# Kernel tuning notes

Measured on AMD Instinct MI355X. Metric: run time of the kernel, lower is better.

The kernel has to match this reference:

```python
import jax, jax.numpy as jnp
import numpy as np

VAR0, VAR1 = 0.1, 0.2
THRESH = 0.5
NEG_POS = 3
NEG_INF = -1e30


def point_form(b):
    # (cx,cy,w,h) -> (x1,y1,x2,y2)
    return jnp.concatenate([b[..., :2] - b[..., 2:] * 0.5,
                            b[..., :2] + b[..., 2:] * 0.5], -1)


def iou(a, b):
    # a: [G,4], b: [A,4], both xyxy -> [G,A]
    tl = jnp.maximum(a[:, None, :2], b[None, :, :2])
    br = jnp.minimum(a[:, None, 2:], b[None, :, 2:])
    wh = jnp.clip(br - tl, 0.0)
    inter = wh[..., 0] * wh[..., 1]
    area_a = (a[:, 2] - a[:, 0]) * (a[:, 3] - a[:, 1])
    area_b = (b[:, 2] - b[:, 0]) * (b[:, 3] - b[:, 1])
    return inter / (area_a[:, None] + area_b[None, :] - inter)


def encode_single(gt_boxes, gt_labels, anchors):
    # gt_boxes [G,4] xyxy, gt_labels [G], anchors [A,4] cxcywh
    ov = iou(gt_boxes, point_form(anchors))            # [G,A]
    best_prior_idx = jnp.argmax(ov, axis=1)            # [G] guaranteed match
    best_truth_ov = jnp.max(ov, axis=0)                # [A]
    best_truth_idx = jnp.argmax(ov, axis=0)            # [A]
    G = gt_boxes.shape[0]
    best_truth_ov = best_truth_ov.at[best_prior_idx].set(2.0)
    best_truth_idx = best_truth_idx.at[best_prior_idx].set(jnp.arange(G))
    matches = gt_boxes[best_truth_idx]                 # [A,4]
    conf = jnp.where(best_truth_ov < THRESH, 0, gt_labels[best_truth_idx] + 1)
    m_cxcy = (matches[:, :2] + matches[:, 2:]) * 0.5
    m_wh = matches[:, 2:] - matches[:, :2]
    g_cxcy = (m_cxcy - anchors[:, :2]) / (VAR0 * anchors[:, 2:])
    g_wh = jnp.log(m_wh / anchors[:, 2:]) / VAR1
    return conf, jnp.concatenate([g_cxcy, g_wh], -1)


def smooth_l1(d):
    ad = jnp.abs(d)
    return jnp.where(ad < 1.0, 0.5 * d * d, ad - 0.5)


def ssd_guarantee_loss(pred_conf, pred_loc, anchors_b, gt_boxes, gt_labels):
    # anchors_b: per-image anchors [B,A,4] (cxcywh)
    conf_t, loc_t = jax.vmap(encode_single)(gt_boxes, gt_labels, anchors_b)
    loc_t = jax.lax.stop_gradient(loc_t)               # loc_t.detach() in torch
    pos = conf_t > 0                                   # [B,A]
    N = jnp.sum(pos).astype(pred_loc.dtype)
    loc_loss = jnp.sum(jnp.where(pos[..., None], smooth_l1(pred_loc - loc_t), 0.0))
    logp = jax.nn.log_softmax(pred_conf, axis=-1)
    ce = -jnp.take_along_axis(logp, conf_t[..., None], axis=-1)[..., 0]  # [B,A]
    A = pred_conf.shape[1]
    pos_num = jnp.sum(pos, axis=1)                     # [B]
    neg_num = jnp.maximum(10, jnp.minimum(pos_num * NEG_POS, A - pos_num))
    neg_ce = jnp.where(conf_t == 0, ce, NEG_INF)
    neg_sorted = -jnp.sort(-neg_ce, axis=1)            # descending hard-negative sort
    rank = jnp.arange(A)
    take = (rank[None, :] < neg_num[:, None]) & (neg_sorted > 0.5 * NEG_INF)
    class_loss = (jnp.sum(jnp.where(pos, ce, 0.0))
                  + jnp.sum(jnp.where(take, neg_sorted, 0.0))) / N
    return class_loss, loc_loss / N, N


def decode(loc, anchors):
    # loc [B,A,4], anchors [A,4] cxcywh -> refined anchors [B,A,4] cxcywh
    cxcy = anchors[None, :, :2] + loc[..., :2] * VAR0 * anchors[None, :, 2:]
    wh = anchors[None, :, 2:] * jnp.exp(loc[..., 2:] * VAR1)
    return jnp.concatenate([cxcy, wh], -1)


def setup_inputs() -> dict:
    key = jax.random.key(0)
    ks = jax.random.split(key, 10)
    B, A, C, G = 32, 16320, 81, 32
    objectness = jax.random.normal(ks[0], (B, A, 2), jnp.float32)
    refine_loc = 0.1 * jax.random.normal(ks[1], (B, A, 4), jnp.float32)
    pred_conf = jax.random.normal(ks[2], (B, A, C), jnp.float32)
    pred_loc = 0.1 * jax.random.normal(ks[3], (B, A, 4), jnp.float32)
    # anchors: valid normalized cxcywh
    a_cxcy = 0.05 + 0.9 * jax.random.uniform(ks[4], (1, A, 2), jnp.float32)
    a_wh = 0.02 + 0.23 * jax.random.uniform(ks[5], (1, A, 2), jnp.float32)
    anchors = jnp.concatenate([a_cxcy, a_wh], -1)
    # gt boxes: valid xyxy in [0,1]
    g_cxcy = 0.2 + 0.6 * jax.random.uniform(ks[6], (B, G, 2), jnp.float32)
    g_wh = 0.05 + 0.25 * jax.random.uniform(ks[7], (B, G, 2), jnp.float32)
    gt_boxes = jnp.clip(jnp.concatenate([g_cxcy - g_wh * 0.5, g_cxcy + g_wh * 0.5], -1), 0.0, 1.0)
    gt_labels = jax.random.randint(ks[8], (B, G), 0, C - 1, jnp.int32)
    return {"objectness": objectness, "refine_loc": refine_loc, "pred_conf": pred_conf,
            "pred_loc": pred_loc, "anchors": anchors, "gt_boxes": gt_boxes,
            "gt_labels": gt_labels}


def reference(objectness, refine_loc, pred_conf, pred_loc, anchors, gt_boxes, gt_labels):
    a0 = anchors[0]                                    # [A,4]
    B = pred_conf.shape[0]
    anchors_b = jnp.broadcast_to(a0, (B,) + a0.shape)
    # ARM: binary objectness, labels zeroed
    arm_cls, arm_loc, _ = ssd_guarantee_loss(objectness, refine_loc, anchors_b,
                                             gt_boxes, jnp.zeros_like(gt_labels))
    # ODM: match against per-image refined anchors
    refined = decode(refine_loc, a0)
    odm_cls, odm_loc, _ = ssd_guarantee_loss(pred_conf, pred_loc, refined,
                                             gt_boxes, gt_labels)
    total = arm_cls + arm_loc + odm_cls + odm_loc
    return (total, odm_cls, odm_loc, arm_cls, arm_loc)
```

## Files before the change

### kernel.cpp

```cpp
#include <hip/hip_runtime.h>
#include <hip/hip_bf16.h>

constexpr int NB = 32;
constexpr int NA = 16320;
constexpr int NG = 32;
constexpr int NC = 81;
constexpr int LSE_BLKS = 2048;
constexpr int CE_BLKS = 2040;

__device__ __forceinline__ float sl1(float d) {
    float ad = fabsf(d);
    return ad < 1.f ? 0.5f * d * d : ad - 0.5f;
}

__device__ __forceinline__ unsigned long long umax64(unsigned long long a, unsigned long long b) {
    return a > b ? a : b;
}

__global__ __launch_bounds__(256) void k_mega(
    const float* __restrict__ anchors,
    const float* __restrict__ refine_loc,
    const float* __restrict__ gt_boxes,
    const float* __restrict__ pred_conf,
    float* __restrict__ lse,
    float* __restrict__ ws_ov,
    unsigned char* __restrict__ ws_idx,
    unsigned long long* __restrict__ ws_part)
{
    __shared__ float4 s_gt[NG];
    __shared__ float s_ga[NG];
    __shared__ unsigned long long s_part[4][NG];

    int bid = blockIdx.x;
    int q = bid / 3, r3 = bid - q * 3;
    int tid = threadIdx.x;

    if (r3 == 0) {
        int lane = tid & 63, sub = lane & 7, grp = lane >> 3;
        int wid = q * 4 + (tid >> 6);
        const int NWAVE = LSE_BLKS * 4;
        const int TOT = NB * NA / 8;
        float x[11]; int idx;
        {
            idx = wid * 8 + grp;
            const float* p = pred_conf + (size_t)idx * NC;
            #pragma unroll
            for (int j = 0; j < 10; j++) x[j] = p[sub + 8 * j];
            x[10] = (sub == 0) ? p[80] : -87.f;
        }
        for (int gi = wid; gi < TOT; gi += NWAVE) {
            float y[11]; int idy = 0;
            int nx = gi + NWAVE;
            if (nx < TOT) {
                idy = nx * 8 + grp;
                const float* p = pred_conf + (size_t)idy * NC;
                #pragma unroll
                for (int j = 0; j < 10; j++) y[j] = p[sub + 8 * j];
                y[10] = (sub == 0) ? p[80] : -87.f;
            } else {
                #pragma unroll
                for (int j = 0; j < 11; j++) y[j] = -87.f;
            }
            float s = __expf(x[10]);
            #pragma unroll
            for (int j = 0; j < 10; j++) s += __expf(x[j]);
            s += __shfl_xor(s, 1);
            s += __shfl_xor(s, 2);
            s += __shfl_xor(s, 4);
            if (sub == 0) lse[idx] = __logf(s);
            #pragma unroll
            for (int j = 0; j < 11; j++) x[j] = y[j];
            idx = idy;
        }
        return;
    }

    int mb = 2 * q + (r3 - 1);
    int row = mb >> 6, chunk = mb & 63;
    int lossId = row >> 5, b = row & 31;
    if (tid < NG) {
        float4 g = *(const float4*)&gt_boxes[(size_t)(b * NG + tid) * 4];
        s_gt[tid] = g;
        s_ga[tid] = (g.z - g.x) * (g.w - g.y);
    }
    __syncthreads();
    int a = chunk * 256 + tid;
    bool valid = a < NA;
    int al = valid ? a : NA - 1;
    float4 an = *(const float4*)&anchors[(size_t)al * 4];
    float acx = an.x, acy = an.y, aw = an.z, ah = an.w;
    if (lossId) {
        float4 rl = *(const float4*)&refine_loc[((size_t)b * NA + al) * 4];
        acx += rl.x * 0.1f * aw;
        acy += rl.y * 0.1f * ah;
        aw *= __expf(rl.z * 0.2f);
        ah *= __expf(rl.w * 0.2f);
    }
    float ax1 = acx - aw * 0.5f, ay1 = acy - ah * 0.5f;
    float ax2 = acx + aw * 0.5f, ay2 = acy + ah * 0.5f;
    float aarea = (ax2 - ax1) * (ay2 - ay1);

    int lane = tid & 63, wv = tid >> 6;
    float best = -1.f; int bg = 0;
    #pragma unroll 1
    for (int g = 0; g < NG; g++) {
        float4 G = s_gt[g];
        float tlx = fmaxf(G.x, ax1);
        float tly = fmaxf(G.y, ay1);
        float brx = fminf(G.z, ax2);
        float bry = fminf(G.w, ay2);
        float w = brx - tlx; w = w > 0.f ? w : 0.f;
        float h = bry - tly; h = h > 0.f ? h : 0.f;
        float inter = w * h;
        float ov = inter * __builtin_amdgcn_rcpf(s_ga[g] + aarea - inter);
        if (!valid) ov = 0.f;
        if (ov > best) { best = ov; bg = g; }
        float m = ov;
        m = fmaxf(m, __shfl_xor(m, 1));
        m = fmaxf(m, __shfl_xor(m, 2));
        m = fmaxf(m, __shfl_xor(m, 4));
        m = fmaxf(m, __shfl_xor(m, 8));
        m = fmaxf(m, __shfl_xor(m, 16));
        m = fmaxf(m, __shfl_xor(m, 32));
        unsigned long long ball = __ballot(ov == m);
        int first = __ffsll((long long)ball) - 1;
        if (lane == 0) {
            unsigned aw_ = (unsigned)(chunk * 256 + wv * 64 + first);
            s_part[wv][g] = ((unsigned long long)__float_as_uint(m) << 32)
                            | (0xFFFFFFFFu - aw_);
        }
    }
    if (valid) {
        size_t sec = (size_t)row * NA;
        ws_ov[sec + a] = best;
        ws_idx[sec + a] = (unsigned char)bg;
    }
    __syncthreads();
    if (tid < NG) {
        unsigned long long k = s_part[0][tid];
        #pragma unroll
        for (int i = 1; i < 4; i++) k = umax64(k, s_part[i][tid]);
        ws_part[(size_t)mb * NG + tid] = k;
    }
}

__global__ __launch_bounds__(256) void k_conf(
    const int* __restrict__ gt_labels,
    const unsigned long long* __restrict__ ws_part,
    const float* __restrict__ ws_ov,
    const unsigned char* __restrict__ ws_idx,
    const float* __restrict__ objectness,
    const float* __restrict__ anchors,
    const float* __restrict__ gt_boxes,
    const float* __restrict__ arm_pred,
    int* __restrict__ match,
    float* __restrict__ negce,
    int* __restrict__ pos_cnt,
    float2* __restrict__ pConf)
{
    int row = blockIdx.x >> 3;
    int chunk = blockIdx.x & 7;
    int lossId = row >> 5, b = row & 31;
    int tid = threadIdx.x;
    __shared__ int s_oa[NG];
    __shared__ int s_lab[NG];
    __shared__ float4 s_gt[NG];
    __shared__ unsigned s_mask[512];
    __shared__ unsigned long long s_pp[8][NG];
    for (int i = tid; i < 512; i += 256) s_mask[i] = 0u;
    {
        int g = tid & 31, s = tid >> 5;
        unsigned long long k = 0ull;
        for (int c = s; c < 64; c += 8)
            k = umax64(k, ws_part[(size_t)(row * 64 + c) * NG + g]);
        s_pp[s][g] = k;
    }
    __syncthreads();
    if (tid < NG) {
        unsigned long long k = s_pp[0][tid];
        #pragma unroll
        for (int i = 1; i < 8; i++) k = umax64(k, s_pp[i][tid]);
        unsigned a = 0xFFFFFFFFu - (unsigned)(k & 0xFFFFFFFFull);
        s_oa[tid] = (int)a;
        s_lab[tid] = lossId ? gt_labels[b * NG + tid] : 0;
        s_gt[tid] = *(const float4*)&gt_boxes[(size_t)(b * NG + tid) * 4];
        atomicOr(&s_mask[a >> 5], 1u << (a & 31));
    }
    __syncthreads();
    size_t sec = (size_t)row * NA;
    int base = chunk * 2040;
    int cnt = 0;
    float pce = 0.f, ploc = 0.f;
    for (int a = base + tid; a < base + 2040; a += 256) {
        float ov = ws_ov[sec + a];
        int g = ws_idx[sec + a];
        if (s_mask[a >> 5] & (1u << (a & 31))) {
            for (int j = NG - 1; j >= 0; j--)
                if (s_oa[j] == a) { g = j; ov = 2.0f; break; }
        }
        int conf = (ov < 0.5f) ? 0 : (s_lab[g] + 1);
        cnt += (conf > 0);
        if (lossId) {
            match[sec + a] = conf | (g << 16);
        } else {
            size_t idx = sec + a;
            float2 x = *(const float2*)&objectness[idx * 2];
            float lse2 = __logf(__expf(x.x) + __expf(x.y));
            float ce = lse2 - (conf ? x.y : x.x);
            if (conf > 0) {
                pce += ce;
                negce[idx] = 0.f;
                float4 an = *(const float4*)&anchors[(size_t)a * 4];
                float4 G = s_gt[g];
                float mcx = (G.x + G.z) * 0.5f, mcy = (G.y + G.w) * 0.5f;
                float mw = G.z - G.x, mh = G.w - G.y;
                float t0 = (mcx - an.x) / (0.1f * an.z);
                float t1 = (mcy - an.y) / (0.1f * an.w);
                float t2 = __logf(mw / an.z) / 0.2f;
                float t3 = __logf(mh / an.w) / 0.2f;
                float4 pl = *(const float4*)&arm_pred[idx * 4];
                ploc += sl1(pl.x - t0) + sl1(pl.y - t1) + sl1(pl.z - t2) + sl1(pl.w - t3);
            } else {
                negce[idx] = ce;
            }
        }
    }
    #pragma unroll
    for (int o = 32; o > 0; o >>= 1) {
        cnt += __shfl_down(cnt, o);
        pce += __shfl_down(pce, o);
        ploc += __shfl_down(ploc, o);
    }
    __shared__ int s_c[4];
    __shared__ float s_p0[4], s_p1[4];
    if ((tid & 63) == 0) {
        int w = tid >> 6;
        s_c[w] = cnt; s_p0[w] = pce; s_p1[w] = ploc;
    }
    __syncthreads();
    if (tid == 0) {
        pos_cnt[blockIdx.x] = s_c[0] + s_c[1] + s_c[2] + s_c[3];
        pConf[blockIdx.x] = make_float2(s_p0[0] + s_p0[1] + s_p0[2] + s_p0[3],
                                        s_p1[0] + s_p1[1] + s_p1[2] + s_p1[3]);
    }
}

__global__ __launch_bounds__(256) void k_ce(
    const float* __restrict__ pred_conf,
    const float* __restrict__ pred_loc,
    const float* __restrict__ anchors,
    const float* __restrict__ refine_loc,
    const float* __restrict__ gt_boxes,
    const int* __restrict__ match,
    const float* __restrict__ lse,
    float* __restrict__ negce,
    float2* __restrict__ partial)
{
    int idx = blockIdx.x * 256 + threadIdx.x;
    int m = match[idx];
    int conf = m & 0xFFFF; int g = m >> 16;
    float xc = pred_conf[(size_t)idx * NC + conf];
    float ce = lse[idx] - xc;
    float pce = 0.f, ploc = 0.f;
    if (conf > 0) {
        pce = ce;
        negce[idx] = 0.f;
        int b = idx / NA, a = idx - b * NA;
        float4 an = *(const float4*)&anchors[(size_t)a * 4];
        float4 rl = *(const float4*)&refine_loc[(size_t)idx * 4];
        float acx = an.x + rl.x * 0.1f * an.z;
        float acy = an.y + rl.y * 0.1f * an.w;
        float aw = an.z * __expf(rl.z * 0.2f);
        float ah = an.w * __expf(rl.w * 0.2f);
        const float* gb = &gt_boxes[(size_t)(b * NG + g) * 4];
        float mcx = (gb[0] + gb[2]) * 0.5f, mcy = (gb[1] + gb[3]) * 0.5f;
        float mw = gb[2] - gb[0], mh = gb[3] - gb[1];
        float t0 = (mcx - acx) / (0.1f * aw);
        float t1 = (mcy - acy) / (0.1f * ah);
        float t2 = __logf(mw / aw) / 0.2f;
        float t3 = __logf(mh / ah) / 0.2f;
        float4 pl = *(const float4*)&pred_loc[(size_t)idx * 4];
        ploc = sl1(pl.x - t0) + sl1(pl.y - t1) + sl1(pl.z - t2) + sl1(pl.w - t3);
    } else {
        negce[idx] = ce;
    }
    #pragma unroll
    for (int o = 32; o > 0; o >>= 1) {
        pce += __shfl_down(pce, o);
        ploc += __shfl_down(ploc, o);
    }
    __shared__ float s0[4], s1[4];
    int w = threadIdx.x >> 6;
    if ((threadIdx.x & 63) == 0) { s0[w] = pce; s1[w] = ploc; }
    __syncthreads();
    if (threadIdx.x == 0) {
        partial[blockIdx.x] = make_float2(s0[0] + s0[1] + s0[2] + s0[3],
                                          s1[0] + s1[1] + s1[2] + s1[3]);
    }
}

__global__ __launch_bounds__(512) void k_topk(
    const float* __restrict__ negce,
    const int* __restrict__ pos_cnt,
    float* __restrict__ topk)
{
    int blk = blockIdx.x;
    int tid = threadIdx.x;
    size_t sec = (size_t)blk * NA;
    float v[32];
    #pragma unroll
    for (int q = 0; q < 32; q++) {
        int i = tid + (q << 9);
        v[q] = (i < NA) ? negce[sec + i] : 0.f;
    }
    __shared__ int s_red[8];
    __shared__ float s_redf[8];
    int p = 0;
    #pragma unroll
    for (int j = 0; j < 8; j++) p += pos_cnt[blk * 8 + j];
    int k = p * 3; if (k > NA - p) k = NA - p; if (k < 10) k = 10;

    unsigned lo = 0u, hi = 0x7F800000u;
    while (lo < hi) {
        unsigned mid = (lo + hi) >> 1;
        float fmid = __uint_as_float(mid);
        int c = 0;
        #pragma unroll
        for (int q = 0; q < 32; q++) c += (v[q] > fmid);
        #pragma unroll
        for (int o = 32; o > 0; o >>= 1) c += __shfl_down(c, o);
        if ((tid & 63) == 0) s_red[tid >> 6] = c;
        __syncthreads();
        int total = 0;
        #pragma unroll
        for (int j = 0; j < 8; j++) total += s_red[j];
        __syncthreads();
        if (total < k) hi = mid; else lo = mid + 1;
    }
    float V = __uint_as_float(lo);
    int c = 0; float sum = 0.f;
    #pragma unroll
    for (int q = 0; q < 32; q++) {
        if (v[q] > V) { c++; sum += v[q]; }
    }
    #pragma unroll
    for (int o = 32; o > 0; o >>= 1) { c += __shfl_down(c, o); sum += __shfl_down(sum, o); }
    if ((tid & 63) == 0) { s_red[tid >> 6] = c; s_redf[tid >> 6] = sum; }
    __syncthreads();
    if (tid == 0) {
        int cg = 0; float sg = 0.f;
        #pragma unroll
        for (int j = 0; j < 8; j++) { cg += s_red[j]; sg += s_redf[j]; }
        topk[blk] = sg + (float)(k - cg) * V;
    }
}

__global__ __launch_bounds__(256) void k_final(
    const float2* __restrict__ pConf, const float2* __restrict__ pOdm,
    const int* __restrict__ pos_cnt, const float* __restrict__ topk,
    float* __restrict__ out)
{
    int tid = threadIdx.x;
    float a0 = 0.f, a1 = 0.f, o0 = 0.f, o1 = 0.f;
    for (int i = tid; i < 512; i += 256) { float2 v = pConf[i]; a0 += v.x; a1 += v.y; }
    for (int i = tid; i < CE_BLKS; i += 256) { float2 v = pOdm[i]; o0 += v.x; o1 += v.y; }
    float n0 = (float)pos_cnt[tid];
    float n1 = (float)pos_cnt[256 + tid];
    float t0 = (tid < NB) ? topk[tid] : 0.f;
    float t1 = (tid < NB) ? topk[NB + tid] : 0.f;
    #pragma unroll
    for (int o = 32; o > 0; o >>= 1) {
        a0 += __shfl_down(a0, o); a1 += __shfl_down(a1, o);
        o0 += __shfl_down(o0, o); o1 += __shfl_down(o1, o);
        n0 += __shfl_down(n0, o); n1 += __shfl_down(n1, o);
        t0 += __shfl_down(t0, o); t1 += __shfl_down(t1, o);
    }
    __shared__ float s[4][8];
    if ((tid & 63) == 0) {
        int w = tid >> 6;
        s[w][0] = a0; s[w][1] = a1; s[w][2] = o0; s[w][3] = o1;
        s[w][4] = n0; s[w][5] = n1; s[w][6] = t0; s[w][7] = t1;
    }
    __syncthreads();
    if (tid == 0) {
        float armce = 0.f, armloc = 0.f, odmce = 0.f, odmloc = 0.f;
        float N0 = 0.f, N1 = 0.f, tk0 = 0.f, tk1 = 0.f;
        #pragma unroll
        for (int i = 0; i < 4; i++) {
            armce += s[i][0]; armloc += s[i][1]; odmce += s[i][2]; odmloc += s[i][3];
            N0 += s[i][4]; N1 += s[i][5]; tk0 += s[i][6]; tk1 += s[i][7];
        }
        float cls0 = (armce + tk0) / N0, loc0 = armloc / N0;
        float cls1 = (odmce + tk1) / N1, loc1 = odmloc / N1;
        out[0] = cls0 + loc0 + cls1 + loc1;
        out[1] = cls1;
        out[2] = loc1;
        out[3] = cls0;
        out[4] = loc0;
    }
}

extern "C" void kernel_launch(void* const* d_in, const int* in_sizes, int n_in,
                              void* d_out, int out_size, void* d_ws, size_t ws_size,
                              hipStream_t stream) {
    const float* objectness = (const float*)d_in[0];
    const float* refine_loc = (const float*)d_in[1];
    const float* pred_conf  = (const float*)d_in[2];
    const float* pred_loc   = (const float*)d_in[3];
    const float* anchors    = (const float*)d_in[4];
    const float* gt_boxes   = (const float*)d_in[5];
    const int*   gt_labels  = (const int*)d_in[6];

    char* w = (char*)d_ws;
    size_t off = 0;
    int* pos_cnt = (int*)(w + off); off += 512 * sizeof(int);
    float* topk = (float*)(w + off); off += 64 * sizeof(float);
    off = (off + 15) & ~(size_t)15;
    float2* pConf = (float2*)(w + off); off += 512 * 8;
    float2* pOdm = (float2*)(w + off); off += (size_t)CE_BLKS * 8;
    unsigned long long* ws_part = (unsigned long long*)(w + off);
    off += (size_t)4096 * NG * 8;
    off = (off + 15) & ~(size_t)15;
    float* lse = (float*)(w + off); off += (size_t)NB * NA * 4;
    float* ws_ov = (float*)(w + off); off += (size_t)2 * NB * NA * 4;
    unsigned char* ws_idx = (unsigned char*)(w + off); off += (size_t)2 * NB * NA;
    off = (off + 15) & ~(size_t)15;
    int* match = (int*)(w + off); off += (size_t)2 * NB * NA * 4;
    float* negce = (float*)(w + off); off += (size_t)2 * NB * NA * 4;

    k_mega<<<3 * 2048, 256, 0, stream>>>(anchors, refine_loc, gt_boxes, pred_conf,
                                         lse, ws_ov, ws_idx, ws_part);
    k_conf<<<64 * 8, 256, 0, stream>>>(gt_labels, ws_part, ws_ov, ws_idx,
                                       objectness, anchors, gt_boxes, refine_loc,
                                       match, negce, pos_cnt, pConf);
    k_ce<<<CE_BLKS, 256, 0, stream>>>(pred_conf, pred_loc, anchors, refine_loc, gt_boxes,
                                      match + (size_t)NB * NA, lse,
                                      negce + (size_t)NB * NA, pOdm);
    k_topk<<<2 * NB, 512, 0, stream>>>(negce, pos_cnt, topk);
    k_final<<<1, 256, 0, stream>>>(pConf, pOdm, pos_cnt, topk, (float*)d_out);
}
```

Measured before the change: 121.2 us.

## Fuse ODM CE/loc into k_conf, compute negative CE inside top-k, fold final reduction

The separate k_ce and k_final kernels are removed. Positive-anchor CE and localization loss for both ARM and ODM are computed directly in k_conf, which now writes only a byte positive mask instead of match and negce arrays. k_topk recomputes the negative CE on the fly from lse, pred_conf and objectness. The last block to finish, found with an atomic counter, performs the final reduction. This removes two launches and large intermediate writes and reads, but adds scattered pred_conf gathers inside top-k and a threadfence/atomic tail step.

```diff
diff --git a/kernel.cpp b/kernel.cpp
--- a/kernel.cpp
+++ b/kernel.cpp
@@ -6,7 +6,6 @@
 constexpr int NG = 32;
 constexpr int NC = 81;
 constexpr int LSE_BLKS = 2048;
-constexpr int CE_BLKS = 2040;
 
 __device__ __forceinline__ float sl1(float d) {
     float ad = fabsf(d);
@@ -150,14 +149,18 @@
     const float* __restrict__ ws_ov,
     const unsigned char* __restrict__ ws_idx,
     const float* __restrict__ objectness,
+    const float* __restrict__ pred_conf,
+    const float* __restrict__ pred_loc,
     const float* __restrict__ anchors,
+    const float* __restrict__ refine_loc,
     const float* __restrict__ gt_boxes,
-    const float* __restrict__ arm_pred,
-    int* __restrict__ match,
-    float* __restrict__ negce,
+    const float* __restrict__ lse,
+    unsigned char* __restrict__ posmask,
     int* __restrict__ pos_cnt,
-    float2* __restrict__ pConf)
+    float2* __restrict__ pConf,
+    unsigned* __restrict__ done_cnt)
 {
+    if (blockIdx.x == 0 && threadIdx.x == 0) *done_cnt = 0u;
     int row = blockIdx.x >> 3;
     int chunk = blockIdx.x & 7;
     int lossId = row >> 5, b = row & 31;
@@ -188,10 +191,11 @@
     }
     __syncthreads();
     size_t sec = (size_t)row * NA;
-    int base = chunk * 2040;
+    int base = chunk * 2048;
+    int lim = (base + 2048 < NA) ? base + 2048 : NA;
     int cnt = 0;
     float pce = 0.f, ploc = 0.f;
-    for (int a = base + tid; a < base + 2040; a += 256) {
+    for (int a = base + tid; a < lim; a += 256) {
         float ov = ws_ov[sec + a];
         int g = ws_idx[sec + a];
         if (s_mask[a >> 5] & (1u << (a & 31))) {
@@ -200,28 +204,35 @@
         }
         int conf = (ov < 0.5f) ? 0 : (s_lab[g] + 1);
         cnt += (conf > 0);
-        if (lossId) {
-            match[sec + a] = conf | (g << 16);
-        } else {
-            size_t idx = sec + a;
-            float2 x = *(const float2*)&objectness[idx * 2];
-            float lse2 = __logf(__expf(x.x) + __expf(x.y));
-            float ce = lse2 - (conf ? x.y : x.x);
-            if (conf > 0) {
-                pce += ce;
-                negce[idx] = 0.f;
-                float4 an = *(const float4*)&anchors[(size_t)a * 4];
-                float4 G = s_gt[g];
-                float mcx = (G.x + G.z) * 0.5f, mcy = (G.y + G.w) * 0.5f;
-                float mw = G.z - G.x, mh = G.w - G.y;
+        posmask[sec + a] = (unsigned char)(conf > 0);
+        if (conf > 0) {
+            size_t gidx = (size_t)b * NA + a;
+            float4 an = *(const float4*)&anchors[(size_t)a * 4];
+            float4 G = s_gt[g];
+            float mcx = (G.x + G.z) * 0.5f, mcy = (G.y + G.w) * 0.5f;
+            float mw = G.z - G.x, mh = G.w - G.y;
+            if (lossId) {
+                pce += lse[gidx] - pred_conf[gidx * NC + conf];
+                float4 rl = *(const float4*)&refine_loc[gidx * 4];
+                float acx = an.x + rl.x * 0.1f * an.z;
+                float acy = an.y + rl.y * 0.1f * an.w;
+                float aw = an.z * __expf(rl.z * 0.2f);
+                float ah = an.w * __expf(rl.w * 0.2f);
+                float t0 = (mcx - acx) / (0.1f * aw);
+                float t1 = (mcy - acy) / (0.1f * ah);
+                float t2 = __logf(mw / aw) / 0.2f;
+                float t3 = __logf(mh / ah) / 0.2f;
+                float4 pl = *(const float4*)&pred_loc[gidx * 4];
+                ploc += sl1(pl.x - t0) + sl1(pl.y - t1) + sl1(pl.z - t2) + sl1(pl.w - t3);
+            } else {
+                float2 x = *(const float2*)&objectness[gidx * 2];
+                pce += __logf(__expf(x.x) + __expf(x.y)) - x.y;
                 float t0 = (mcx - an.x) / (0.1f * an.z);
                 float t1 = (mcy - an.y) / (0.1f * an.w);
                 float t2 = __logf(mw / an.z) / 0.2f;
                 float t3 = __logf(mh / an.w) / 0.2f;
-                float4 pl = *(const float4*)&arm_pred[idx * 4];
+                float4 pl = *(const float4*)&refine_loc[gidx * 4];
                 ploc += sl1(pl.x - t0) + sl1(pl.y - t1) + sl1(pl.z - t2) + sl1(pl.w - t3);
-            } else {
-                negce[idx] = ce;
             }
         }
     }
@@ -245,79 +256,42 @@
     }
 }
 
-__global__ __launch_bounds__(256) void k_ce(
+__global__ __launch_bounds__(512) void k_topk(
+    const float* __restrict__ objectness,
     const float* __restrict__ pred_conf,
-    const float* __restrict__ pred_loc,
-    const float* __restrict__ anchors,
-    const float* __restrict__ refine_loc,
-    const float* __restrict__ gt_boxes,
-    const int* __restrict__ match,
     const float* __restrict__ lse,
-    float* __restrict__ negce,
-    float2* __restrict__ partial)
+    const unsigned char* __restrict__ posmask,
+    const int* __restrict__ pos_cnt,
+    const float2* __restrict__ pConf,
+    float* __restrict__ topk,
+    unsigned* __restrict__ done_cnt,
+    float* __restrict__ out)
 {
-    int idx = blockIdx.x * 256 + threadIdx.x;
-    int m = match[idx];
-    int conf = m & 0xFFFF; int g = m >> 16;
-    float xc = pred_conf[(size_t)idx * NC + conf];
-    float ce = lse[idx] - xc;
-    float pce = 0.f, ploc = 0.f;
-    if (conf > 0) {
-        pce = ce;
-        negce[idx] = 0.f;
-        int b = idx / NA, a = idx - b * NA;
-        float4 an = *(const float4*)&anchors[(size_t)a * 4];
-        float4 rl = *(const float4*)&refine_loc[(size_t)idx * 4];
-        float acx = an.x + rl.x * 0.1f * an.z;
-        float acy = an.y + rl.y * 0.1f * an.w;
-        float aw = an.z * __expf(rl.z * 0.2f);
-        float ah = an.w * __expf(rl.w * 0.2f);
-        const float* gb = &gt_boxes[(size_t)(b * NG + g) * 4];
-        float mcx = (gb[0] + gb[2]) * 0.5f, mcy = (gb[1] + gb[3]) * 0.5f;
-        float mw = gb[2] - gb[0], mh = gb[3] - gb[1];
-        float t0 = (mcx - acx) / (0.1f * aw);
-        float t1 = (mcy - acy) / (0.1f * ah);
-        float t2 = __logf(mw / aw) / 0.2f;
-        float t3 = __logf(mh / ah) / 0.2f;
-        float4 pl = *(const float4*)&pred_loc[(size_t)idx * 4];
-        ploc = sl1(pl.x - t0) + sl1(pl.y - t1) + sl1(pl.z - t2) + sl1(pl.w - t3);
-    } else {
-        negce[idx] = ce;
-    }
-    #pragma unroll
-    for (int o = 32; o > 0; o >>= 1) {
-        pce += __shfl_down(pce, o);
-        ploc += __shfl_down(ploc, o);
-    }
-    __shared__ float s0[4], s1[4];
-    int w = threadIdx.x >> 6;
-    if ((threadIdx.x & 63) == 0) { s0[w] = pce; s1[w] = ploc; }
-    __syncthreads();
-    if (threadIdx.x == 0) {
-        partial[blockIdx.x] = make_float2(s0[0] + s0[1] + s0[2] + s0[3],
-                                          s1[0] + s1[1] + s1[2] + s1[3]);
-    }
-}
-
-__global__ __launch_bounds__(512) void k_topk(
-    const float* __restrict__ negce,
-    const int* __restrict__ pos_cnt,
-    float* __restrict__ topk)
-{
-    int blk = blockIdx.x;
+    int row = blockIdx.x;
+    int lossId = row >> 5, b = row & 31;
     int tid = threadIdx.x;
-    size_t sec = (size_t)blk * NA;
+    size_t sec = (size_t)row * NA;
     float v[32];
     #pragma unroll
     for (int q = 0; q < 32; q++) {
-        int i = tid + (q << 9);
-        v[q] = (i < NA) ? negce[sec + i] : 0.f;
+        int a = tid + (q << 9);
+        float ce = 0.f;
+        if (a < NA && !posmask[sec + a]) {
+            size_t gidx = (size_t)b * NA + a;
+            if (lossId) {
+                ce = lse[gidx] - pred_conf[gidx * NC];
+            } else {
+                float2 x = *(const float2*)&objectness[gidx * 2];
+                ce = __logf(__expf(x.x) + __expf(x.y)) - x.x;
+            }
+        }
+        v[q] = ce;
     }
     __shared__ int s_red[8];
     __shared__ float s_redf[8];
     int p = 0;
     #pragma unroll
-    for (int j = 0; j < 8; j++) p += pos_cnt[blk * 8 + j];
+    for (int j = 0; j < 8; j++) p += pos_cnt[row * 8 + j];
     int k = p * 3; if (k > NA - p) k = NA - p; if (k < 10) k = 10;
 
     unsigned lo = 0u, hi = 0x7F800000u;
@@ -351,23 +325,22 @@
         int cg = 0; float sg = 0.f;
         #pragma unroll
         for (int j = 0; j < 8; j++) { cg += s_red[j]; sg += s_redf[j]; }
-        topk[blk] = sg + (float)(k - cg) * V;
-    }
-}
-
-__global__ __launch_bounds__(256) void k_final(
-    const float2* __restrict__ pConf, const float2* __restrict__ pOdm,
-    const int* __restrict__ pos_cnt, const float* __restrict__ topk,
-    float* __restrict__ out)
-{
-    int tid = threadIdx.x;
-    float a0 = 0.f, a1 = 0.f, o0 = 0.f, o1 = 0.f;
-    for (int i = tid; i < 512; i += 256) { float2 v = pConf[i]; a0 += v.x; a1 += v.y; }
-    for (int i = tid; i < CE_BLKS; i += 256) { float2 v = pOdm[i]; o0 += v.x; o1 += v.y; }
-    float n0 = (float)pos_cnt[tid];
-    float n1 = (float)pos_cnt[256 + tid];
+        topk[row] = sg + (float)(k - cg) * V;
+    }
+    __threadfence();
+    __shared__ unsigned s_t;
+    if (tid == 0) s_t = atomicAdd(done_cnt, 1u);
+    __syncthreads();
+    if (s_t != 63u) return;
+
+    bool arm = tid < 256;
+    float2 pc = pConf[tid];
+    float a0 = arm ? pc.x : 0.f, a1 = arm ? pc.y : 0.f;
+    float o0 = arm ? 0.f : pc.x, o1 = arm ? 0.f : pc.y;
+    float n0 = arm ? (float)pos_cnt[tid] : 0.f;
+    float n1 = arm ? 0.f : (float)pos_cnt[tid];
     float t0 = (tid < NB) ? topk[tid] : 0.f;
-    float t1 = (tid < NB) ? topk[NB + tid] : 0.f;
+    float t1 = (tid >= NB && tid < 2 * NB) ? topk[tid] : 0.f;
     #pragma unroll
     for (int o = 32; o > 0; o >>= 1) {
         a0 += __shfl_down(a0, o); a1 += __shfl_down(a1, o);
@@ -375,7 +348,7 @@
         n0 += __shfl_down(n0, o); n1 += __shfl_down(n1, o);
         t0 += __shfl_down(t0, o); t1 += __shfl_down(t1, o);
     }
-    __shared__ float s[4][8];
+    __shared__ float s[8][8];
     if ((tid & 63) == 0) {
         int w = tid >> 6;
         s[w][0] = a0; s[w][1] = a1; s[w][2] = o0; s[w][3] = o1;
@@ -386,7 +359,7 @@
         float armce = 0.f, armloc = 0.f, odmce = 0.f, odmloc = 0.f;
         float N0 = 0.f, N1 = 0.f, tk0 = 0.f, tk1 = 0.f;
         #pragma unroll
-        for (int i = 0; i < 4; i++) {
+        for (int i = 0; i < 8; i++) {
             armce += s[i][0]; armloc += s[i][1]; odmce += s[i][2]; odmloc += s[i][3];
             N0 += s[i][4]; N1 += s[i][5]; tk0 += s[i][6]; tk1 += s[i][7];
         }
@@ -415,27 +388,23 @@
     size_t off = 0;
     int* pos_cnt = (int*)(w + off); off += 512 * sizeof(int);
     float* topk = (float*)(w + off); off += 64 * sizeof(float);
+    unsigned* done_cnt = (unsigned*)(w + off); off += 16;
     off = (off + 15) & ~(size_t)15;
     float2* pConf = (float2*)(w + off); off += 512 * 8;
-    float2* pOdm = (float2*)(w + off); off += (size_t)CE_BLKS * 8;
     unsigned long long* ws_part = (unsigned long long*)(w + off);
     off += (size_t)4096 * NG * 8;
     off = (off + 15) & ~(size_t)15;
     float* lse = (float*)(w + off); off += (size_t)NB * NA * 4;
     float* ws_ov = (float*)(w + off); off += (size_t)2 * NB * NA * 4;
     unsigned char* ws_idx = (unsigned char*)(w + off); off += (size_t)2 * NB * NA;
-    off = (off + 15) & ~(size_t)15;
-    int* match = (int*)(w + off); off += (size_t)2 * NB * NA * 4;
-    float* negce = (float*)(w + off); off += (size_t)2 * NB * NA * 4;
+    unsigned char* posmask = (unsigned char*)(w + off); off += (size_t)2 * NB * NA;
 
     k_mega<<<3 * 2048, 256, 0, stream>>>(anchors, refine_loc, gt_boxes, pred_conf,
                                          lse, ws_ov, ws_idx, ws_part);
     k_conf<<<64 * 8, 256, 0, stream>>>(gt_labels, ws_part, ws_ov, ws_idx,
-                                       objectness, anchors, gt_boxes, refine_loc,
-                                       match, negce, pos_cnt, pConf);
-    k_ce<<<CE_BLKS, 256, 0, stream>>>(pred_conf, pred_loc, anchors, refine_loc, gt_boxes,
-                                      match + (size_t)NB * NA, lse,
-                                      negce + (size_t)NB * NA, pOdm);
-    k_topk<<<2 * NB, 512, 0, stream>>>(negce, pos_cnt, topk);
-    k_final<<<1, 256, 0, stream>>>(pConf, pOdm, pos_cnt, topk, (float*)d_out);
-}
+                                       objectness, pred_conf, pred_loc, anchors,
+                                       refine_loc, gt_boxes, lse,
+                                       posmask, pos_cnt, pConf, done_cnt);
+    k_topk<<<64, 512, 0, stream>>>(objectness, pred_conf, lse, posmask, pos_cnt,
+                                   pConf, topk, done_cnt, (float*)d_out);
+}
```

New measurement: 136.9 us. +13.0%, slower.
